# Kernel tuning notes

Measured on AMD Instinct MI355X. Metric: run time of the kernel, lower is better.

Reference implementation:

```python
import jax, jax.numpy as jnp
import numpy as np

NA, NB, MAXNB = 100000, 200000, 6
ATOM_FDIM, BOND_FDIM, H, DEPTH = 133, 147, 300, 3


def setup_inputs() -> dict:
    key = jax.random.key(0)
    ks = jax.random.split(key, 8)
    # index 0 is the zero-padding entry (chemprop convention)
    f_atoms = jax.random.normal(ks[0], (NA, ATOM_FDIM), jnp.float32).at[0].set(0.0)
    f_bonds = jax.random.normal(ks[1], (NB, BOND_FDIM), jnp.float32).at[0].set(0.0)
    a2b = jax.random.randint(ks[2], (NA, MAXNB), 0, NB)
    b2a = jax.random.randint(ks[3], (NB,), 0, NA)
    b2revb = jax.random.randint(ks[4], (NB,), 0, NB)
    W_i = jax.random.normal(ks[5], (BOND_FDIM, H), jnp.float32) * (1.0 / np.sqrt(BOND_FDIM))
    W_h = jax.random.normal(ks[6], (H, H), jnp.float32) * (1.0 / np.sqrt(H))
    W_o = jax.random.normal(ks[7], (ATOM_FDIM + H, H), jnp.float32) * (1.0 / np.sqrt(ATOM_FDIM + H))
    b_o = jnp.zeros((H,), jnp.float32)
    return {"f_atoms": f_atoms, "f_bonds": f_bonds, "a2b": a2b, "b2a": b2a,
            "b2revb": b2revb, "W_i": W_i, "W_h": W_h, "W_o": W_o, "b_o": b_o}


def reference(f_atoms, f_bonds, a2b, b2a, b2revb, W_i, W_h, W_o, b_o):
    # bond-message D-MPNN forward (atom_messages=False, attention=False,
    # undirected=False, dropout=0 / eval mode)
    inp = f_bonds @ W_i                     # [NB, H]
    message = jax.nn.relu(inp)              # [NB, H]
    for _ in range(DEPTH - 1):
        # gather incoming bond messages per atom and sum over neighbors
        a_message = message[a2b].sum(axis=1)          # [NA, MAXNB, H] -> [NA, H]
        message = a_message[b2a] - message[b2revb]    # [NB, H]
        message = jax.nn.relu(inp + message @ W_h)
    a_message = message[a2b].sum(axis=1)              # [NA, H]
    a_input = jnp.concatenate([f_atoms, a_message], axis=1)  # [NA, ATOM_FDIM+H]
    atom_hiddens = jax.nn.relu(a_input @ W_o + b_o)   # [NA, H]
    # the per-molecule narrow loop in the original merely re-slices
    # atom_hiddens by a_scope; the concatenation of all slices == atom_hiddens
    return atom_hiddens
```

## Files before the change

### kernel.cpp

```cpp
#include <hip/hip_runtime.h>
#include <hip/hip_fp16.h>

#define NA 100000
#define NB 200000
#define MAXNB 6
#define AF 133
#define BF 147
#define H 300
#define HP 320
#define AFP 160
#define NP 320
#define KP_C 480
#define BM 128
#define BN 320
#define BK 32
#define NTH 512
#define LDK 40

typedef _Float16 f16;
typedef __attribute__((ext_vector_type(8))) _Float16 f16x8;
typedef __attribute__((ext_vector_type(4))) float f32x4;

__global__ void conv_pad_f16(const float* __restrict__ src, f16* __restrict__ dst,
                             int M, int Ks) {
  int idx = blockIdx.x * blockDim.x + threadIdx.x;
  if (idx >= M * (AFP / 8)) return;
  int r = idx / (AFP / 8);
  int c = (idx - r * (AFP / 8)) * 8;
  f16x8 o;
#pragma unroll
  for (int j = 0; j < 8; ++j) {
    int k = c + j;
    o[j] = (k < Ks) ? (f16)src[(size_t)r * Ks + k] : (f16)0.0f;
  }
  *(f16x8*)&dst[(size_t)r * AFP + c] = o;
}

__global__ void prep_w1(const float* __restrict__ Wi, const float* __restrict__ Wh,
                        f16* __restrict__ dst) {
  int idx = blockIdx.x * blockDim.x + threadIdx.x;
  if (idx >= NP * KP_C) return;
  int n = idx / KP_C, k = idx - n * KP_C;
  float v = 0.0f;
  if (n < H) {
    if (k < BF) v = Wi[(size_t)k * H + n];
    else if (k >= AFP && k < AFP + H) v = Wh[(size_t)(k - AFP) * H + n];
  }
  dst[idx] = (f16)v;
}

__global__ void prep_wo(const float* __restrict__ src, f16* __restrict__ dst) {
  int idx = blockIdx.x * blockDim.x + threadIdx.x;
  if (idx >= NP * KP_C) return;
  int n = idx / KP_C, k = idx - n * KP_C;
  int ks = -1;
  if (k < AF) ks = k;
  else if (k >= AFP && k < AFP + H) ks = AF + (k - AFP);
  float v = (n < H && ks >= 0) ? src[(size_t)ks * H + n] : 0.0f;
  dst[idx] = (f16)v;
}

__global__ void gather_sum_kernel(const f16* __restrict__ msg,
                                  const int* __restrict__ a2b,
                                  f16* __restrict__ amsg) {
  int idx = blockIdx.x * blockDim.x + threadIdx.x;
  if (idx >= NA * (HP / 8)) return;
  int a = idx / (HP / 8);
  int c = (idx - a * (HP / 8)) * 8;
  const int* nbr = &a2b[(size_t)a * MAXNB];
  float acc[8] = {0.f, 0.f, 0.f, 0.f, 0.f, 0.f, 0.f, 0.f};
#pragma unroll
  for (int t = 0; t < MAXNB; ++t) {
    int r = nbr[t];
    f16x8 v = *(const f16x8*)&msg[(size_t)r * HP + c];
#pragma unroll
    for (int j = 0; j < 8; ++j) acc[j] += (float)v[j];
  }
  f16x8 o;
#pragma unroll
  for (int j = 0; j < 8; ++j) o[j] = (f16)acc[j];
  *(f16x8*)&amsg[(size_t)a * HP + c] = o;
}

template <int MODE>
__global__ __launch_bounds__(NTH)
void gemm_kernel(const f16* __restrict__ Afp,
                 const f16* __restrict__ amsg,
                 const f16* __restrict__ msg_in,
                 const int* __restrict__ b2a,
                 const int* __restrict__ b2revb,
                 const int* __restrict__ a2b,
                 const f16* __restrict__ Wp,
                 const float* __restrict__ b_o,
                 f16* __restrict__ out_msg,
                 float* __restrict__ out_f32) {
  constexpr int KSTEPS = (MODE == 0) ? 5 : 15;
  constexpr int ASTEPS = 5;
  constexpr int M = (MODE == 2) ? NA : NB;

  __shared__ f16 As[2][BM][LDK];
  __shared__ f16 Bs[2][BN][LDK];

  const int mb = blockIdx.x;
  const int tid = threadIdx.x;
  const int lane = tid & 63, wid = tid >> 6;
  const int wr = wid >> 2, wc = wid & 3;

  f32x4 acc[4][5] = {};

  const int arow = tid >> 2;
  const int ac = (tid & 3) * 8;
  const int m_g = mb * BM + arow;
  const int mrow = (m_g < M) ? m_g : 0;

  const int bidx2 = tid + 2 * NTH;
  const int br0 = tid >> 2,            bc0 = (tid & 3) * 8;
  const int br1 = (tid + NTH) >> 2,    bc1 = ((tid + NTH) & 3) * 8;
  const int br2 = bidx2 >> 2,          bc2 = (bidx2 & 3) * 8;
  const bool b2ok = bidx2 < BN * 4;

  int ra = 0, rb = 0;
  int n0 = 0, n1 = 0, n2 = 0, n3 = 0, n4 = 0, n5 = 0;
  if constexpr (MODE == 1) { ra = b2a[mrow]; rb = b2revb[mrow]; }
  if constexpr (MODE == 2) {
    const int* p = &a2b[(size_t)mrow * MAXNB];
    n0 = p[0]; n1 = p[1]; n2 = p[2]; n3 = p[3]; n4 = p[4]; n5 = p[5];
  }

  f16x8 axA, ayA, avA[6];
  f16x8 axB, ayB, avB[6];
  f16x8 pw0, pw1, pw2;

  auto issueA = [&](int ks, f16x8& ax, f16x8& ay, f16x8 (&av)[6]) {
    const int kb = ks * BK + ac;
    if constexpr (MODE == 0) {
      ax = *(const f16x8*)&Afp[(size_t)mrow * AFP + kb];
    } else if constexpr (MODE == 1) {
      if (ks < ASTEPS) {
        ax = *(const f16x8*)&Afp[(size_t)mrow * AFP + kb];
      } else {
        const int kk = kb - AFP;
        ax = *(const f16x8*)&amsg[(size_t)ra * HP + kk];
        ay = *(const f16x8*)&msg_in[(size_t)rb * HP + kk];
      }
    } else {
      if (ks < ASTEPS) {
        ax = *(const f16x8*)&Afp[(size_t)mrow * AFP + kb];
      } else {
        const int kk = kb - AFP;
        av[0] = *(const f16x8*)&msg_in[(size_t)n0 * HP + kk];
        av[1] = *(const f16x8*)&msg_in[(size_t)n1 * HP + kk];
        av[2] = *(const f16x8*)&msg_in[(size_t)n2 * HP + kk];
        av[3] = *(const f16x8*)&msg_in[(size_t)n3 * HP + kk];
        av[4] = *(const f16x8*)&msg_in[(size_t)n4 * HP + kk];
        av[5] = *(const f16x8*)&msg_in[(size_t)n5 * HP + kk];
      }
    }
  };

  auto issueB = [&](int ks) {
    const int kw = ks * BK;
    pw0 = *(const f16x8*)&Wp[(size_t)br0 * KP_C + kw + bc0];
    pw1 = *(const f16x8*)&Wp[(size_t)br1 * KP_C + kw + bc1];
    if (b2ok) pw2 = *(const f16x8*)&Wp[(size_t)br2 * KP_C + kw + bc2];
  };

  auto write_lds = [&](int buf, int ks, f16x8& ax, f16x8& ay, f16x8 (&av)[6]) {
    f16x8 pa = ax;
    if constexpr (MODE == 1) {
      if (ks >= ASTEPS) pa = ax - ay;
    }
    if constexpr (MODE == 2) {
      if (ks >= ASTEPS) pa = ((av[0] + av[1]) + (av[2] + av[3])) + (av[4] + av[5]);
    }
    *(f16x8*)&As[buf][arow][ac] = pa;
    *(f16x8*)&Bs[buf][br0][bc0] = pw0;
    *(f16x8*)&Bs[buf][br1][bc1] = pw1;
    if (b2ok) *(f16x8*)&Bs[buf][br2][bc2] = pw2;
  };

  const int row16 = lane & 15, kh = (lane >> 4) * 8;

  auto compute = [&](int buf) {
    f16x8 af[4], bfr[5];
#pragma unroll
    for (int m = 0; m < 4; ++m)
      af[m] = *(const f16x8*)&As[buf][wr * 64 + m * 16 + row16][kh];
#pragma unroll
    for (int n = 0; n < 5; ++n)
      bfr[n] = *(const f16x8*)&Bs[buf][wc * 80 + n * 16 + row16][kh];
#pragma unroll
    for (int m = 0; m < 4; ++m)
#pragma unroll
      for (int n = 0; n < 5; ++n)
        acc[m][n] = __builtin_amdgcn_mfma_f32_16x16x32_f16(af[m], bfr[n], acc[m][n], 0, 0, 0);
  };

  issueA(0, axA, ayA, avA); issueB(0);
  write_lds(0, 0, axA, ayA, avA);
  issueA(1, axB, ayB, avB); issueB(1);
  __syncthreads();

  for (int ks = 0; ks < KSTEPS; ks += 2) {
    if (ks + 2 < KSTEPS) issueA(ks + 2, axA, ayA, avA);
    compute(0);
    if (ks + 1 < KSTEPS) write_lds(1, ks + 1, axB, ayB, avB);
    if (ks + 2 < KSTEPS) issueB(ks + 2);
    __syncthreads();
    if (ks + 1 < KSTEPS) {
      if (ks + 3 < KSTEPS) issueA(ks + 3, axB, ayB, avB);
      compute(1);
      if (ks + 2 < KSTEPS) write_lds(0, ks + 2, axA, ayA, avA);
      if (ks + 3 < KSTEPS) issueB(ks + 3);
      __syncthreads();
    }
  }

  const int rquad = (lane >> 4) * 4;
#pragma unroll
  for (int m = 0; m < 4; ++m) {
#pragma unroll
    for (int n = 0; n < 5; ++n) {
      const int col = wc * 80 + n * 16 + row16;
#pragma unroll
      for (int j = 0; j < 4; ++j) {
        const int row = mb * BM + wr * 64 + m * 16 + rquad + j;
        float v = acc[m][n][j];
        if constexpr (MODE == 2) {
          if (row < M && col < H)
            out_f32[(size_t)row * H + col] = fmaxf(v + b_o[col], 0.0f);
        } else {
          if (row < M)
            out_msg[(size_t)row * HP + col] = (f16)fmaxf(v, 0.0f);
        }
      }
    }
  }
}

extern "C" void kernel_launch(void* const* d_in, const int* in_sizes, int n_in,
                              void* d_out, int out_size, void* d_ws, size_t ws_size,
                              hipStream_t stream) {
  const float* f_atoms = (const float*)d_in[0];
  const float* f_bonds = (const float*)d_in[1];
  const int*   a2b     = (const int*)d_in[2];
  const int*   b2a     = (const int*)d_in[3];
  const int*   b2revb  = (const int*)d_in[4];
  const float* W_i     = (const float*)d_in[5];
  const float* W_h     = (const float*)d_in[6];
  const float* W_o     = (const float*)d_in[7];
  const float* b_o     = (const float*)d_in[8];
  float* out = (float*)d_out;

  char* ws = (char*)d_ws;
  size_t off = 0;
  f16* msgA = (f16*)(ws + off); off += (size_t)NB * HP * 2;
  f16* msgB = (f16*)(ws + off); off += (size_t)NB * HP * 2;
  f16* amsg = (f16*)(ws + off); off += (size_t)NA * HP * 2;
  f16* fb16 = (f16*)(ws + off); off += (size_t)NB * AFP * 2;
  f16* fa16 = (f16*)(ws + off); off += (size_t)NA * AFP * 2;
  f16* W1P  = (f16*)(ws + off); off += (size_t)NP * KP_C * 2;
  f16* WoP  = (f16*)(ws + off); off += (size_t)NP * KP_C * 2;
  if (off > ws_size) return;

  prep_w1<<<(NP * KP_C + 255) / 256, 256, 0, stream>>>(W_i, W_h, W1P);
  prep_wo<<<(NP * KP_C + 255) / 256, 256, 0, stream>>>(W_o, WoP);
  conv_pad_f16<<<(NB * (AFP / 8) + 255) / 256, 256, 0, stream>>>(f_bonds, fb16, NB, BF);
  conv_pad_f16<<<(NA * (AFP / 8) + 255) / 256, 256, 0, stream>>>(f_atoms, fa16, NA, AF);

  const int gB = (NB + BM - 1) / BM;
  const int gA = (NA + BM - 1) / BM;
  dim3 gS((NA * (HP / 8) + 255) / 256);

  gemm_kernel<0><<<gB, NTH, 0, stream>>>(fb16, nullptr, nullptr,
                                         nullptr, nullptr, nullptr, W1P, nullptr,
                                         msgA, nullptr);
  gather_sum_kernel<<<gS, 256, 0, stream>>>(msgA, a2b, amsg);
  gemm_kernel<1><<<gB, NTH, 0, stream>>>(fb16, amsg, msgA,
                                         b2a, b2revb, nullptr, W1P, nullptr,
                                         msgB, nullptr);
  gather_sum_kernel<<<gS, 256, 0, stream>>>(msgB, a2b, amsg);
  gemm_kernel<1><<<gB, NTH, 0, stream>>>(fb16, amsg, msgB,
                                         b2a, b2revb, nullptr, W1P, nullptr,
                                         msgA, nullptr);
  gemm_kernel<2><<<gA, NTH, 0, stream>>>(fa16, nullptr, msgA,
                                         nullptr, nullptr, a2b, WoP, b_o,
                                         nullptr, out);
}
```

Before: 687.6 us.

## Prelayout weights in MFMA fragment order and load B directly from global

Result: slower. 707.8 us (+2.9%).

```diff
diff --git a/kernel.cpp b/kernel.cpp
--- a/kernel.cpp
+++ b/kernel.cpp
@@ -16,6 +16,7 @@
 #define BK 32
 #define NTH 512
 #define LDK 40
+#define NFRAG 20
 
 typedef _Float16 f16;
 typedef __attribute__((ext_vector_type(8))) _Float16 f16x8;
@@ -36,11 +37,14 @@
   *(f16x8*)&dst[(size_t)r * AFP + c] = o;
 }
 
-__global__ void prep_w1(const float* __restrict__ Wi, const float* __restrict__ Wh,
-                        f16* __restrict__ dst) {
+__global__ void prep_w1frag(const float* __restrict__ Wi, const float* __restrict__ Wh,
+                            f16* __restrict__ dst) {
   int idx = blockIdx.x * blockDim.x + threadIdx.x;
   if (idx >= NP * KP_C) return;
-  int n = idx / KP_C, k = idx - n * KP_C;
+  int j = idx & 7, lane = (idx >> 3) & 63, frag = idx >> 9;
+  int ks = frag / NFRAG, nf = frag - ks * NFRAG;
+  int n = nf * 16 + (lane & 15);
+  int k = ks * 32 + ((lane >> 4) * 8) + j;
   float v = 0.0f;
   if (n < H) {
     if (k < BF) v = Wi[(size_t)k * H + n];
@@ -49,14 +53,17 @@
   dst[idx] = (f16)v;
 }
 
-__global__ void prep_wo(const float* __restrict__ src, f16* __restrict__ dst) {
+__global__ void prep_wofrag(const float* __restrict__ src, f16* __restrict__ dst) {
   int idx = blockIdx.x * blockDim.x + threadIdx.x;
   if (idx >= NP * KP_C) return;
-  int n = idx / KP_C, k = idx - n * KP_C;
-  int ks = -1;
-  if (k < AF) ks = k;
-  else if (k >= AFP && k < AFP + H) ks = AF + (k - AFP);
-  float v = (n < H && ks >= 0) ? src[(size_t)ks * H + n] : 0.0f;
+  int j = idx & 7, lane = (idx >> 3) & 63, frag = idx >> 9;
+  int ks = frag / NFRAG, nf = frag - ks * NFRAG;
+  int n = nf * 16 + (lane & 15);
+  int k = ks * 32 + ((lane >> 4) * 8) + j;
+  int kk = -1;
+  if (k < AF) kk = k;
+  else if (k >= AFP && k < AFP + H) kk = AF + (k - AFP);
+  float v = (n < H && kk >= 0) ? src[(size_t)kk * H + n] : 0.0f;
   dst[idx] = (f16)v;
 }
 
@@ -90,7 +97,7 @@
                  const int* __restrict__ b2a,
                  const int* __restrict__ b2revb,
                  const int* __restrict__ a2b,
-                 const f16* __restrict__ Wp,
+                 const f16* __restrict__ Wf,
                  const float* __restrict__ b_o,
                  f16* __restrict__ out_msg,
                  float* __restrict__ out_f32) {
@@ -99,7 +106,6 @@
   constexpr int M = (MODE == 2) ? NA : NB;
 
   __shared__ f16 As[2][BM][LDK];
-  __shared__ f16 Bs[2][BN][LDK];
 
   const int mb = blockIdx.x;
   const int tid = threadIdx.x;
@@ -112,12 +118,6 @@
   const int ac = (tid & 3) * 8;
   const int m_g = mb * BM + arow;
   const int mrow = (m_g < M) ? m_g : 0;
-
-  const int bidx2 = tid + 2 * NTH;
-  const int br0 = tid >> 2,            bc0 = (tid & 3) * 8;
-  const int br1 = (tid + NTH) >> 2,    bc1 = ((tid + NTH) & 3) * 8;
-  const int br2 = bidx2 >> 2,          bc2 = (bidx2 & 3) * 8;
-  const bool b2ok = bidx2 < BN * 4;
 
   int ra = 0, rb = 0;
   int n0 = 0, n1 = 0, n2 = 0, n3 = 0, n4 = 0, n5 = 0;
@@ -129,7 +129,6 @@
 
   f16x8 axA, ayA, avA[6];
   f16x8 axB, ayB, avB[6];
-  f16x8 pw0, pw1, pw2;
 
   auto issueA = [&](int ks, f16x8& ax, f16x8& ay, f16x8 (&av)[6]) {
     const int kb = ks * BK + ac;
@@ -158,13 +157,6 @@
     }
   };
 
-  auto issueB = [&](int ks) {
-    const int kw = ks * BK;
-    pw0 = *(const f16x8*)&Wp[(size_t)br0 * KP_C + kw + bc0];
-    pw1 = *(const f16x8*)&Wp[(size_t)br1 * KP_C + kw + bc1];
-    if (b2ok) pw2 = *(const f16x8*)&Wp[(size_t)br2 * KP_C + kw + bc2];
-  };
-
   auto write_lds = [&](int buf, int ks, f16x8& ax, f16x8& ay, f16x8 (&av)[6]) {
     f16x8 pa = ax;
     if constexpr (MODE == 1) {
@@ -174,21 +166,19 @@
       if (ks >= ASTEPS) pa = ((av[0] + av[1]) + (av[2] + av[3])) + (av[4] + av[5]);
     }
     *(f16x8*)&As[buf][arow][ac] = pa;
-    *(f16x8*)&Bs[buf][br0][bc0] = pw0;
-    *(f16x8*)&Bs[buf][br1][bc1] = pw1;
-    if (b2ok) *(f16x8*)&Bs[buf][br2][bc2] = pw2;
   };
 
   const int row16 = lane & 15, kh = (lane >> 4) * 8;
 
-  auto compute = [&](int buf) {
+  auto compute = [&](int buf, int ks) {
+    const f16* wp = Wf + ((size_t)ks * NFRAG + wc * 5) * 512 + (size_t)lane * 8;
     f16x8 af[4], bfr[5];
+#pragma unroll
+    for (int n = 0; n < 5; ++n)
+      bfr[n] = *(const f16x8*)(wp + n * 512);
 #pragma unroll
     for (int m = 0; m < 4; ++m)
       af[m] = *(const f16x8*)&As[buf][wr * 64 + m * 16 + row16][kh];
-#pragma unroll
-    for (int n = 0; n < 5; ++n)
-      bfr[n] = *(const f16x8*)&Bs[buf][wc * 80 + n * 16 + row16][kh];
 #pragma unroll
     for (int m = 0; m < 4; ++m)
 #pragma unroll
@@ -196,22 +186,20 @@
         acc[m][n] = __builtin_amdgcn_mfma_f32_16x16x32_f16(af[m], bfr[n], acc[m][n], 0, 0, 0);
   };
 
-  issueA(0, axA, ayA, avA); issueB(0);
+  issueA(0, axA, ayA, avA);
   write_lds(0, 0, axA, ayA, avA);
-  issueA(1, axB, ayB, avB); issueB(1);
+  issueA(1, axB, ayB, avB);
   __syncthreads();
 
   for (int ks = 0; ks < KSTEPS; ks += 2) {
     if (ks + 2 < KSTEPS) issueA(ks + 2, axA, ayA, avA);
-    compute(0);
+    compute(0, ks);
     if (ks + 1 < KSTEPS) write_lds(1, ks + 1, axB, ayB, avB);
-    if (ks + 2 < KSTEPS) issueB(ks + 2);
     __syncthreads();
     if (ks + 1 < KSTEPS) {
       if (ks + 3 < KSTEPS) issueA(ks + 3, axB, ayB, avB);
-      compute(1);
+      compute(1, ks + 1);
       if (ks + 2 < KSTEPS) write_lds(0, ks + 2, axA, ayA, avA);
-      if (ks + 3 < KSTEPS) issueB(ks + 3);
       __syncthreads();
     }
   }
@@ -259,12 +247,12 @@
   f16* amsg = (f16*)(ws + off); off += (size_t)NA * HP * 2;
   f16* fb16 = (f16*)(ws + off); off += (size_t)NB * AFP * 2;
   f16* fa16 = (f16*)(ws + off); off += (size_t)NA * AFP * 2;
-  f16* W1P  = (f16*)(ws + off); off += (size_t)NP * KP_C * 2;
-  f16* WoP  = (f16*)(ws + off); off += (size_t)NP * KP_C * 2;
+  f16* W1F  = (f16*)(ws + off); off += (size_t)NP * KP_C * 2;
+  f16* WoF  = (f16*)(ws + off); off += (size_t)NP * KP_C * 2;
   if (off > ws_size) return;
 
-  prep_w1<<<(NP * KP_C + 255) / 256, 256, 0, stream>>>(W_i, W_h, W1P);
-  prep_wo<<<(NP * KP_C + 255) / 256, 256, 0, stream>>>(W_o, WoP);
+  prep_w1frag<<<(NP * KP_C + 255) / 256, 256, 0, stream>>>(W_i, W_h, W1F);
+  prep_wofrag<<<(NP * KP_C + 255) / 256, 256, 0, stream>>>(W_o, WoF);
   conv_pad_f16<<<(NB * (AFP / 8) + 255) / 256, 256, 0, stream>>>(f_bonds, fb16, NB, BF);
   conv_pad_f16<<<(NA * (AFP / 8) + 255) / 256, 256, 0, stream>>>(f_atoms, fa16, NA, AF);
 
@@ -273,17 +261,17 @@
   dim3 gS((NA * (HP / 8) + 255) / 256);
 
   gemm_kernel<0><<<gB, NTH, 0, stream>>>(fb16, nullptr, nullptr,
-                                         nullptr, nullptr, nullptr, W1P, nullptr,
+                                         nullptr, nullptr, nullptr, W1F, nullptr,
                                          msgA, nullptr);
   gather_sum_kernel<<<gS, 256, 0, stream>>>(msgA, a2b, amsg);
   gemm_kernel<1><<<gB, NTH, 0, stream>>>(fb16, amsg, msgA,
-                                         b2a, b2revb, nullptr, W1P, nullptr,
+                                         b2a, b2revb, nullptr, W1F, nullptr,
                                          msgB, nullptr);
   gather_sum_kernel<<<gS, 256, 0, stream>>>(msgB, a2b, amsg);
   gemm_kernel<1><<<gB, NTH, 0, stream>>>(fb16, amsg, msgB,
-                                         b2a, b2revb, nullptr, W1P, nullptr,
+                                         b2a, b2revb, nullptr, W1F, nullptr,
                                          msgA, nullptr);
   gemm_kernel<2><<<gA, NTH, 0, stream>>>(fa16, nullptr, msgA,
-                                         nullptr, nullptr, a2b, WoP, b_o,
+                                         nullptr, nullptr, a2b, WoF, b_o,
                                          nullptr, out);
 }
```
